# Kernel tuning notes

Measured on AMD Instinct MI355X. Metric: run time of the kernel, lower is better.

The kernel has to match this reference:

```python
import jax, jax.numpy as jnp
import numpy as np

N, E, D, H, A = 50000, 800000, 128, 256, 16


def setup_inputs() -> dict:
    key = jax.random.key(0)
    ks = jax.random.split(key, 16)
    s = 0.05
    return {
        "x": jax.random.normal(ks[0], (N, D), jnp.float32),
        "edge_index": jax.random.randint(ks[1], (2, E), 0, N, dtype=jnp.int32),
        "edge_attr": jax.random.normal(ks[2], (E, A), jnp.float32),
        # GCNConv 1 (input_dim -> hidden_dim): lin weight (no bias) + conv bias
        "W1": jax.random.normal(ks[3], (D, H), jnp.float32) * s,
        "b1": jnp.zeros((H,), jnp.float32),
        # GCNConv 2 (hidden_dim -> input_dim)
        "W2": jax.random.normal(ks[4], (H, D), jnp.float32) * s,
        "b2": jnp.zeros((D,), jnp.float32),
        # output_layer MLP: D -> H -> D
        "Wo1": jax.random.normal(ks[5], (D, H), jnp.float32) * s,
        "bo1": jnp.zeros((H,), jnp.float32),
        "Wo2": jax.random.normal(ks[6], (H, D), jnp.float32) * s,
        "bo2": jnp.zeros((D,), jnp.float32),
        # edge_predictor MLP: 2D+A -> H -> A
        "We1": jax.random.normal(ks[7], (2 * D + A, H), jnp.float32) * s,
        "be1": jnp.zeros((H,), jnp.float32),
        "We2": jax.random.normal(ks[8], (H, A), jnp.float32) * s,
        "be2": jnp.zeros((A,), jnp.float32),
    }


def reference(x, edge_index, edge_attr, W1, b1, W2, b2, Wo1, bo1, Wo2, bo2,
              We1, be1, We2, be2):
    n = x.shape[0]
    row, col = edge_index[0], edge_index[1]
    # GCNConv default: add self-loops, symmetric normalization deg^-1/2 A deg^-1/2
    loop = jnp.arange(n, dtype=row.dtype)
    row_f = jnp.concatenate([row, loop])
    col_f = jnp.concatenate([col, loop])
    deg = jax.ops.segment_sum(jnp.ones_like(col_f, dtype=x.dtype), col_f,
                              num_segments=n)
    dinv = jnp.where(deg > 0, jax.lax.rsqrt(jnp.maximum(deg, 1.0)), 0.0)
    norm = dinv[row_f] * dinv[col_f]  # [E+N]

    def gcn(h, W, b):
        h = h @ W                                # [n, out]
        msg = h[row_f] * norm[:, None]           # gather + scale
        agg = jax.ops.segment_sum(msg, col_f, num_segments=n)  # scatter-add
        return agg + b

    h = jax.nn.relu(gcn(x, W1, b1))
    h = jax.nn.relu(gcn(h, W2, b2))
    h = jax.nn.relu(h @ Wo1 + bo1) @ Wo2 + bo2   # output_layer MLP

    # edge predictor: gather endpoint features, concat with edge_attr, MLP
    edge_input = jnp.concatenate([h[row], h[col], edge_attr], axis=1)
    ea = jax.nn.relu(edge_input @ We1 + be1) @ We2 + be2
    return h, ea
```

## Files before the change

### kernel.cpp

```cpp
#include <hip/hip_runtime.h>
#include <hip/hip_bf16.h>

#define N_NODES 50000
#define N_EDGES 800000
#define DIM_D   128
#define DIM_H   256
#define DIM_A   16

typedef unsigned short u16;
typedef __attribute__((ext_vector_type(4))) float f4;
typedef __attribute__((ext_vector_type(8))) short s8;
typedef __attribute__((ext_vector_type(4))) short s4;

__device__ __forceinline__ u16 f2bf(float f) {
    union { float f; unsigned u; } v; v.f = f;
    unsigned r = v.u + 0x7FFFu + ((v.u >> 16) & 1u);
    return (u16)(r >> 16);
}
__device__ __forceinline__ float bf2f(u16 s) {
    union { unsigned u; float f; } v; v.u = ((unsigned)s) << 16; return v.f;
}
__device__ __forceinline__ s8 zero_s8() {
    s8 v;
#pragma unroll
    for (int i = 0; i < 8; i++) v[i] = 0;
    return v;
}

__device__ __forceinline__ int pq_off(int mt, int q) {
    return (mt >> 2) * 64 + ((mt >> 1) & 1) * 32 + q * 8 + (mt & 1) * 4;
}

__global__ __launch_bounds__(256) void k_zero(int* __restrict__ cnt) {
    int i = blockIdx.x * 256 + threadIdx.x;
    if (i < N_NODES) cnt[i] = 0;
}
__global__ __launch_bounds__(256) void k_count(const int* __restrict__ coli, int* __restrict__ cnt) {
    int e = blockIdx.x * 256 + threadIdx.x;
    if (e < N_EDGES) atomicAdd(&cnt[coli[e]], 1);
}
__global__ __launch_bounds__(256) void k_dinv(const int* __restrict__ cnt, float* __restrict__ dinv) {
    int i = blockIdx.x * 256 + threadIdx.x;
    if (i < N_NODES) dinv[i] = rsqrtf((float)(cnt[i] + 1));
}

#define SCAN_C 49
__global__ __launch_bounds__(1024) void k_scan(const int* __restrict__ cnt, int* __restrict__ start) {
    __shared__ int ps[1024];
    int t = threadIdx.x;
    int base = t * SCAN_C;
    int sum = 0;
    for (int i = 0; i < SCAN_C; i++) {
        int idx = base + i;
        sum += (idx < N_NODES) ? cnt[idx] : 0;
    }
    ps[t] = sum;
    __syncthreads();
    for (int ofs = 1; ofs < 1024; ofs <<= 1) {
        int v = (t >= ofs) ? ps[t - ofs] : 0;
        __syncthreads();
        ps[t] += v;
        __syncthreads();
    }
    int run = (t > 0) ? ps[t - 1] : 0;
    for (int i = 0; i < SCAN_C; i++) {
        int idx = base + i;
        if (idx < N_NODES) {
            start[idx] = run;
            run += cnt[idx];
        }
    }
    if (t == 1023) start[N_NODES] = ps[1023];
}
__global__ __launch_bounds__(256) void k_copy(const int* __restrict__ start, int* __restrict__ cursor) {
    int i = blockIdx.x * 256 + threadIdx.x;
    if (i < N_NODES) cursor[i] = start[i];
}
__global__ __launch_bounds__(256) void k_fill(const int* __restrict__ rowi, const int* __restrict__ coli,
                                              const float* __restrict__ dinv,
                                              int* __restrict__ cursor, int2* __restrict__ pack,
                                              int2* __restrict__ eidx) {
    int e = blockIdx.x * 256 + threadIdx.x;
    if (e >= N_EDGES) return;
    int r = rowi[e], c = coli[e];
    int slot = atomicAdd(&cursor[c], 1);
    float w = dinv[r] * dinv[c];
    pack[slot] = make_int2(r, __float_as_int(w));
    eidx[slot] = make_int2(e, c);
}

__global__ __launch_bounds__(256) void k_cast(const float* __restrict__ X, u16* __restrict__ Y, int n4) {
    int i = blockIdx.x * 256 + threadIdx.x;
    if (i >= n4) return;
    float4 v = *(const float4*)&X[(size_t)i * 4];
    ushort4 o;
    o.x = f2bf(v.x); o.y = f2bf(v.y); o.z = f2bf(v.z); o.w = f2bf(v.w);
    *(ushort4*)&Y[(size_t)i * 4] = o;
}

__global__ __launch_bounds__(256) void k_gather(const u16* __restrict__ X,
                                                const int2* __restrict__ pack,
                                                const int* __restrict__ start,
                                                const float* __restrict__ dinv,
                                                float* __restrict__ z) {
    int node = blockIdx.x * 4 + (threadIdx.x >> 6);
    if (node >= N_NODES) return;
    int lane = threadIdx.x & 63;
    int half = lane >> 5, j = lane & 31;
    int c4 = j * 4;
    float di = dinv[node];
    f4 acc = {0.f, 0.f, 0.f, 0.f};
    if (half == 0) {
        float sl = di * di;
        ushort4 u = *(const ushort4*)&X[(size_t)node * DIM_D + c4];
        acc[0] = bf2f(u.x) * sl; acc[1] = bf2f(u.y) * sl;
        acc[2] = bf2f(u.z) * sl; acc[3] = bf2f(u.w) * sl;
    }
    int s = start[node], e = start[node + 1];
#pragma unroll 8
    for (int i = s + half; i < e; i += 2) {
        int2 p = pack[i];
        float w = __int_as_float(p.y);
        ushort4 u = *(const ushort4*)&X[(size_t)p.x * DIM_D + c4];
        acc[0] += bf2f(u.x) * w; acc[1] += bf2f(u.y) * w;
        acc[2] += bf2f(u.z) * w; acc[3] += bf2f(u.w) * w;
    }
    float t0 = acc[0] + __shfl(acc[0], j + 32);
    float t1 = acc[1] + __shfl(acc[1], j + 32);
    float t2 = acc[2] + __shfl(acc[2], j + 32);
    float t3 = acc[3] + __shfl(acc[3], j + 32);
    if (half == 0)
        *(float4*)&z[(size_t)node * DIM_D + c4] = make_float4(t0, t1, t2, t3);
}

__global__ __launch_bounds__(256) void k_twt(const float* __restrict__ W, u16* __restrict__ Wt,
                                             int K, int Nn) {
    int idx = blockIdx.x * 256 + threadIdx.x;
    if (idx >= K * Nn) return;
    int k = idx / Nn, n = idx - k * Nn;
    Wt[n * K + k] = f2bf(W[idx]);
}

__global__ __launch_bounds__(256) void k_bpq(const float* __restrict__ be1, float* __restrict__ bpq) {
    int i = blockIdx.x * 256 + threadIdx.x;
    if (i < 512) bpq[i] = (i < 256) ? be1[i] : 0.f;
}

#define BM 128
#define BN 64
#define BK 32
#define BKP 56

template <bool A_BF16, bool PRE_BR, bool POST_RELU, bool OUT_BF16, bool PERM_PQ>
__global__ __launch_bounds__(256) void k_gemm(const void* __restrict__ Ap,
                                              const u16* __restrict__ Wt,
                                              const float* __restrict__ preB,
                                              const float* __restrict__ postB,
                                              void* __restrict__ Cp,
                                              int M, int K, int Nn) {
    __shared__ __align__(16) u16 As[BM * BKP];
    __shared__ __align__(16) u16 Bs[BN * BKP];
    const int tid = threadIdx.x;
    const int wid = tid >> 6, lane = tid & 63;
    const int q = lane >> 4, l = lane & 15;
    const int bm = blockIdx.x * BM, bn = blockIdx.y * BN;

    f4 acc[8];
#pragma unroll
    for (int i = 0; i < 8; i++) { f4 zz = {0.f, 0.f, 0.f, 0.f}; acc[i] = zz; }

    for (int k0 = 0; k0 < K; k0 += BK) {
        __syncthreads();
        {
            int n = tid >> 2, kc = (tid & 3) * 8;
            *(int4*)&Bs[n * BKP + kc] = *(const int4*)&Wt[(size_t)(bn + n) * K + k0 + kc];
        }
        if (A_BF16) {
            const u16* A = (const u16*)Ap;
#pragma unroll
            for (int p = 0; p < 2; p++) {
                int m = (tid >> 2) + p * 64, kc = (tid & 3) * 8;
                int gm = bm + m; if (gm >= M) gm = M - 1;
                *(int4*)&As[m * BKP + kc] = *(const int4*)&A[(size_t)gm * K + k0 + kc];
            }
        } else {
            const float* A = (const float*)Ap;
#pragma unroll
            for (int p = 0; p < 4; p++) {
                int m = (tid >> 3) + p * 32, k4 = (tid & 7) * 4;
                int gm = bm + m; if (gm >= M) gm = M - 1;
                float4 v = *(const float4*)&A[(size_t)gm * K + k0 + k4];
                if (PRE_BR) {
                    const float4 pb = *(const float4*)&preB[k0 + k4];
                    v.x = fmaxf(v.x + pb.x, 0.f);
                    v.y = fmaxf(v.y + pb.y, 0.f);
                    v.z = fmaxf(v.z + pb.z, 0.f);
                    v.w = fmaxf(v.w + pb.w, 0.f);
                }
                ushort4 o;
                o.x = f2bf(v.x); o.y = f2bf(v.y); o.z = f2bf(v.z); o.w = f2bf(v.w);
                *(ushort4*)&As[m * BKP + k4] = o;
            }
        }
        __syncthreads();

        s8 af[2], bf[4];
#pragma unroll
        for (int mt = 0; mt < 2; mt++)
            af[mt] = *(const s8*)&As[(wid * 32 + mt * 16 + l) * BKP + q * 8];
#pragma unroll
        for (int nt = 0; nt < 4; nt++)
            bf[nt] = *(const s8*)&Bs[(nt * 16 + l) * BKP + q * 8];
#pragma unroll
        for (int mt = 0; mt < 2; mt++)
#pragma unroll
            for (int nt = 0; nt < 4; nt++)
                acc[mt * 4 + nt] = __builtin_amdgcn_mfma_f32_16x16x32_bf16(
                    af[mt], bf[nt], acc[mt * 4 + nt], 0, 0, 0);
    }

#pragma unroll
    for (int mt = 0; mt < 2; mt++) {
#pragma unroll
        for (int nt = 0; nt < 4; nt++) {
            int colg = bn + nt * 16 + l;
            float pb = postB ? postB[colg] : 0.0f;
            int cols = colg;
            if (PERM_PQ) {
                int w = colg & 63, mtL = w >> 4;
                cols = (colg & ~63) | (((mtL >> 1) & 1) * 32) | (((w >> 2) & 3) * 8)
                       | ((mtL & 1) * 4) | (w & 3);
            }
#pragma unroll
            for (int r = 0; r < 4; r++) {
                int rowg = bm + wid * 32 + mt * 16 + q * 4 + r;
                if (rowg < M) {
                    float v = acc[mt * 4 + nt][r] + pb;
                    if (POST_RELU) v = fmaxf(v, 0.f);
                    if (OUT_BF16)
                        ((u16*)Cp)[(size_t)rowg * Nn + cols] = f2bf(v);
                    else
                        ((float*)Cp)[(size_t)rowg * Nn + cols] = v;
                }
            }
        }
    }
}

#if __has_builtin(__builtin_amdgcn_mfma_f32_16x16x16bf16_1k)
#define KEEP4(a,b,c,d) asm volatile("" :: "v"(a), "v"(b), "v"(c), "v"(d))
__global__ __launch_bounds__(256) void k_edge(const u16* __restrict__ PQ,
                                              const float* __restrict__ attr,
                                              const int2* __restrict__ pack,
                                              const int2* __restrict__ eidx,
                                              const u16* __restrict__ Wct,
                                              const u16* __restrict__ We2t,
                                              const float* __restrict__ be2,
                                              float* __restrict__ outp) {
    const int tid = threadIdx.x, wid = tid >> 6, lane = tid & 63;
    const int q = lane >> 4, l = lane & 15;
    const float4 be2v = *(const float4*)&be2[q * 4];
    const int NT = N_EDGES / 16;
    const int step = gridDim.x * 4;

    s4 we2f[16], wcf[16];
#pragma unroll
    for (int mt = 0; mt < 16; mt++) {
        we2f[mt] = *(const s4*)&We2t[(size_t)l * DIM_H + mt * 16 + q * 4];
        wcf[mt]  = *(const s4*)&Wct[(mt * 16 + l) * 16 + q * 4];
    }

    int tile = blockIdx.x * 4 + wid;
    if (tile >= NT) return;
    int2 pk = pack[tile * 16 + l];
    int2 ec = eidx[tile * 16 + l];

    for (; tile < NT; tile += step) {
        const int re = pk.x, e = ec.x, ce = ec.y;
        const u16* prow = PQ + (size_t)re * 512 + q * 8;
        const u16* qrow = PQ + (size_t)ce * 512 + 256 + q * 8;

        float4 av = *(const float4*)&attr[(size_t)e * DIM_A + q * 4];
        s8 pw[8], qw[8];
#pragma unroll
        for (int w = 0; w < 8; w++) {
            pw[w] = *(const s8*)(prow + w * 32);
            qw[w] = *(const s8*)(qrow + w * 32);
        }
        int ntile = tile + step;
        int ns = (ntile < NT) ? ntile * 16 + l : l;
        int2 pk_n = pack[ns];
        int2 ec_n = eidx[ns];
        KEEP4(pw[0], pw[1], pw[2], pw[3]);
        KEEP4(pw[4], pw[5], pw[6], pw[7]);
        KEEP4(qw[0], qw[1], qw[2], qw[3]);
        KEEP4(qw[4], qw[5], qw[6], qw[7]);
        __builtin_amdgcn_sched_barrier(0);

        s4 af;
        af[0] = (short)f2bf(av.x); af[1] = (short)f2bf(av.y);
        af[2] = (short)f2bf(av.z); af[3] = (short)f2bf(av.w);

        f4 acc2 = {0.f, 0.f, 0.f, 0.f};
#pragma unroll
        for (int w = 0; w < 8; w++) {
#pragma unroll
            for (int s = 0; s < 2; s++) {
                const int mt = w * 2 + s;
                f4 cz = {0.f, 0.f, 0.f, 0.f};
                f4 acc = __builtin_amdgcn_mfma_f32_16x16x16bf16_1k(wcf[mt], af, cz, 0, 0, 0);
                float t0 = bf2f((u16)pw[w][s * 4 + 0]) + bf2f((u16)qw[w][s * 4 + 0]) + acc[0];
                float t1 = bf2f((u16)pw[w][s * 4 + 1]) + bf2f((u16)qw[w][s * 4 + 1]) + acc[1];
                float t2 = bf2f((u16)pw[w][s * 4 + 2]) + bf2f((u16)qw[w][s * 4 + 2]) + acc[2];
                float t3 = bf2f((u16)pw[w][s * 4 + 3]) + bf2f((u16)qw[w][s * 4 + 3]) + acc[3];
                s4 uf;
                uf[0] = (short)f2bf(fmaxf(t0, 0.f));
                uf[1] = (short)f2bf(fmaxf(t1, 0.f));
                uf[2] = (short)f2bf(fmaxf(t2, 0.f));
                uf[3] = (short)f2bf(fmaxf(t3, 0.f));
                acc2 = __builtin_amdgcn_mfma_f32_16x16x16bf16_1k(we2f[mt], uf, acc2, 0, 0, 0);
            }
        }
        *(float4*)&outp[(size_t)e * DIM_A + q * 4] =
            make_float4(acc2[0] + be2v.x, acc2[1] + be2v.y,
                        acc2[2] + be2v.z, acc2[3] + be2v.w);
        pk = pk_n; ec = ec_n;
    }
}
#else
#define UPAD 268
__global__ __launch_bounds__(256) void k_edge(const u16* __restrict__ PQ,
                                              const float* __restrict__ attr,
                                              const int2* __restrict__ pack,
                                              const int2* __restrict__ eidx,
                                              const u16* __restrict__ Wct,
                                              const u16* __restrict__ We2t,
                                              const float* __restrict__ be2,
                                              float* __restrict__ outp) {
    __shared__ __align__(16) u16 ub[4][16][UPAD];
    const int tid = threadIdx.x, wid = tid >> 6, lane = tid & 63;
    const int q = lane >> 4, l = lane & 15;
    const float4 be2v = *(const float4*)&be2[q * 4];
    u16(*u)[UPAD] = ub[wid];

    s8 wcf[16];
#pragma unroll
    for (int mt = 0; mt < 16; mt++) {
        wcf[mt] = zero_s8();
        if (q < 2) wcf[mt] = *(const s8*)&Wct[(mt * 16 + l) * 16 + q * 8];
    }

    for (int tile = blockIdx.x * 4 + wid; tile < N_EDGES / 16; tile += gridDim.x * 4) {
        const int s = tile * 16 + l;
        const int2 pk = pack[s];
        const int2 ec = eidx[s];
        const int re = pk.x, e = ec.x, ce = ec.y;
        const u16* prow = PQ + (size_t)re * 512;
        const u16* qrow = PQ + (size_t)ce * 512 + 256;

        s8 af = zero_s8();
        if (q < 2) {
            const float* ap = &attr[(size_t)e * DIM_A + q * 8];
            float4 a0 = *(const float4*)ap;
            float4 a1 = *(const float4*)(ap + 4);
            af[0] = (short)f2bf(a0.x); af[1] = (short)f2bf(a0.y);
            af[2] = (short)f2bf(a0.z); af[3] = (short)f2bf(a0.w);
            af[4] = (short)f2bf(a1.x); af[5] = (short)f2bf(a1.y);
            af[6] = (short)f2bf(a1.z); af[7] = (short)f2bf(a1.w);
        }

#pragma unroll
        for (int mt = 0; mt < 16; mt++) {
            f4 cz = {0.f, 0.f, 0.f, 0.f};
            f4 acc = __builtin_amdgcn_mfma_f32_16x16x32_bf16(wcf[mt], af, cz, 0, 0, 0);
            ushort4 pu = *(const ushort4*)(prow + pq_off(mt, q));
            ushort4 qu = *(const ushort4*)(qrow + pq_off(mt, q));
            float t0 = bf2f(pu.x) + bf2f(qu.x) + acc[0];
            float t1 = bf2f(pu.y) + bf2f(qu.y) + acc[1];
            float t2 = bf2f(pu.z) + bf2f(qu.z) + acc[2];
            float t3 = bf2f(pu.w) + bf2f(qu.w) + acc[3];
            ushort4 o;
            o.x = f2bf(fmaxf(t0, 0.f)); o.y = f2bf(fmaxf(t1, 0.f));
            o.z = f2bf(fmaxf(t2, 0.f)); o.w = f2bf(fmaxf(t3, 0.f));
            *(ushort4*)&u[l][mt * 16 + q * 4] = o;
        }

        f4 acc2 = {0.f, 0.f, 0.f, 0.f};
#pragma unroll
        for (int ks = 0; ks < 8; ks++) {
            s8 uf = *(const s8*)&u[l][ks * 32 + q * 8];
            s8 wf = *(const s8*)&We2t[(size_t)l * DIM_H + ks * 32 + q * 8];
            acc2 = __builtin_amdgcn_mfma_f32_16x16x32_bf16(wf, uf, acc2, 0, 0, 0);
        }
        *(float4*)&outp[(size_t)e * DIM_A + q * 4] =
            make_float4(acc2[0] + be2v.x, acc2[1] + be2v.y,
                        acc2[2] + be2v.z, acc2[3] + be2v.w);
    }
}
#endif

extern "C" void kernel_launch(void* const* d_in, const int* in_sizes, int n_in,
                              void* d_out, int out_size, void* d_ws, size_t ws_size,
                              hipStream_t stream) {
    (void)in_sizes; (void)n_in; (void)out_size; (void)ws_size;
    const float* x    = (const float*)d_in[0];
    const int*   ei   = (const int*)d_in[1];
    const float* attr = (const float*)d_in[2];
    const float* W1   = (const float*)d_in[3];
    const float* b1   = (const float*)d_in[4];
    const float* W2   = (const float*)d_in[5];
    const float* b2   = (const float*)d_in[6];
    const float* Wo1  = (const float*)d_in[7];
    const float* bo1  = (const float*)d_in[8];
    const float* Wo2  = (const float*)d_in[9];
    const float* bo2  = (const float*)d_in[10];
    const float* We1  = (const float*)d_in[11];
    const float* be1  = (const float*)d_in[12];
    const float* We2  = (const float*)d_in[13];
    const float* be2  = (const float*)d_in[14];
    const int* rowi = ei;
    const int* coli = ei + N_EDGES;

    float* hout = (float*)d_out;
    float* eout = hout + (size_t)N_NODES * DIM_D;

    char* ws = (char*)d_ws;
    size_t off = 0;
    auto nxt = [&](size_t b) -> void* {
        void* p = ws + off; off = (off + b + 255) & ~(size_t)255; return p;
    };
    float* dinv = (float*)nxt((size_t)N_NODES * 4);
    int* cnt    = (int*)nxt((size_t)N_NODES * 4);
    int* startp = (int*)nxt((size_t)(N_NODES + 1) * 4);
    int* cursor = (int*)nxt((size_t)N_NODES * 4);
    int2* pack  = (int2*)nxt((size_t)N_EDGES * 8);
    int2* eidx  = (int2*)nxt((size_t)N_EDGES * 8);
    u16* W1t   = (u16*)nxt(128 * 256 * 2);
    u16* W2t   = (u16*)nxt(128 * 256 * 2);
    u16* Wo1t  = (u16*)nxt(128 * 256 * 2);
    u16* Wo2t  = (u16*)nxt(128 * 256 * 2);
    u16* Wabt  = (u16*)nxt(512 * 128 * 2);
    u16* Wct   = (u16*)nxt(256 * 16 * 2);
    u16* We2t  = (u16*)nxt(16 * 256 * 2);
    float* bpq = (float*)nxt(512 * 4);
    u16* xb    = (u16*)nxt((size_t)N_NODES * DIM_D * 2);
    float* z   = (float*)nxt((size_t)N_NODES * DIM_D * 4);
    u16* h1    = (u16*)nxt((size_t)N_NODES * DIM_H * 2);
    u16* yb    = (u16*)nxt((size_t)N_NODES * DIM_D * 2);
    u16* PQb = (u16*)z;

    const int gN = (N_NODES + 255) / 256;
    const int gE = (N_EDGES + 255) / 256;

    k_twt<<<(128 * 256 + 255) / 256, 256, 0, stream>>>(W1, W1t, 128, 256);
    k_twt<<<(128 * 256 + 255) / 256, 256, 0, stream>>>(W2, W2t, 256, 128);
    k_twt<<<(128 * 256 + 255) / 256, 256, 0, stream>>>(Wo1, Wo1t, 128, 256);
    k_twt<<<(128 * 256 + 255) / 256, 256, 0, stream>>>(Wo2, Wo2t, 256, 128);
    k_twt<<<(128 * 256 + 255) / 256, 256, 0, stream>>>(We1, Wabt, 128, 256);
    k_twt<<<(128 * 256 + 255) / 256, 256, 0, stream>>>(We1 + 128 * 256, Wabt + 256 * 128, 128, 256);
    k_twt<<<(16 * 256 + 255) / 256, 256, 0, stream>>>(We1 + 256 * 256, Wct, 16, 256);
    k_twt<<<(16 * 256 + 255) / 256, 256, 0, stream>>>(We2, We2t, 256, 16);
    k_bpq<<<2, 256, 0, stream>>>(be1, bpq);

    k_zero<<<gN, 256, 0, stream>>>(cnt);
    k_count<<<gE, 256, 0, stream>>>(coli, cnt);
    k_dinv<<<gN, 256, 0, stream>>>(cnt, dinv);
    k_scan<<<1, 1024, 0, stream>>>(cnt, startp);
    k_copy<<<gN, 256, 0, stream>>>(startp, cursor);
    k_fill<<<gE, 256, 0, stream>>>(rowi, coli, dinv, cursor, pack, eidx);

    k_cast<<<(N_NODES * DIM_D / 4 + 255) / 256, 256, 0, stream>>>(x, xb, N_NODES * DIM_D / 4);

    dim3 g4(391, 4), g2(391, 2), g8(391, 8);
    const int gG = (N_NODES + 3) / 4;
    k_gather<<<gG, 256, 0, stream>>>(xb, pack, startp, dinv, z);
    k_gemm<false, false, true, true, false><<<g4, 256, 0, stream>>>(z, W1t, nullptr, b1, h1, N_NODES, 128, 256);
    k_gemm<true, false, false, true, false><<<g2, 256, 0, stream>>>(h1, W2t, nullptr, nullptr, yb, N_NODES, 256, 128);
    k_gather<<<gG, 256, 0, stream>>>(yb, pack, startp, dinv, z);
    k_gemm<false, true, true, true, false><<<g4, 256, 0, stream>>>(z, Wo1t, b2, bo1, h1, N_NODES, 128, 256);
    k_gemm<true, false, false, false, false><<<g2, 256, 0, stream>>>(h1, Wo2t, nullptr, bo2, hout, N_NODES, 256, 128);
    k_gemm<false, false, false, true, true><<<g8, 256, 0, stream>>>(hout, Wabt, nullptr, bpq, PQb, N_NODES, 128, 512);
    k_edge<<<2048, 256, 0, stream>>>(PQb, attr, pack, eidx, Wct, We2t, be2, eout);
}
```

Baseline: 681.2 us.

## Split gather edge ranges per half-wave, stage edge MLP weights in LDS

The GCN gather kernel now gives each half-wave a contiguous half of the node's edge range and unrolls by four with loads issued ahead of the FMAs, raising memory-level parallelism. The edge kernel moves the 32 per-lane weight fragments from registers into shared memory and reads them per MFMA, cutting VGPR pressure to allow more waves in flight. It also feeds the P+Q sum straight in as the MFMA accumulator input, removing separate adds. The cost is extra LDS reads inside the hot loop.

New measurement: 667.1 us. -2.1%, faster.

```diff
diff --git a/kernel.cpp b/kernel.cpp
--- a/kernel.cpp
+++ b/kernel.cpp
@@ -116,9 +116,28 @@
         acc[0] = bf2f(u.x) * sl; acc[1] = bf2f(u.y) * sl;
         acc[2] = bf2f(u.z) * sl; acc[3] = bf2f(u.w) * sl;
     }
-    int s = start[node], e = start[node + 1];
-#pragma unroll 8
-    for (int i = s + half; i < e; i += 2) {
+    int s0 = start[node], e0 = start[node + 1];
+    int h0 = (e0 - s0 + 1) >> 1;
+    int i   = half ? (s0 + h0) : s0;
+    int end = half ? e0 : (s0 + h0);
+    for (; i + 3 < end; i += 4) {
+        int2 p0 = pack[i], p1 = pack[i + 1], p2 = pack[i + 2], p3 = pack[i + 3];
+        ushort4 u0 = *(const ushort4*)&X[(size_t)p0.x * DIM_D + c4];
+        ushort4 u1 = *(const ushort4*)&X[(size_t)p1.x * DIM_D + c4];
+        ushort4 u2 = *(const ushort4*)&X[(size_t)p2.x * DIM_D + c4];
+        ushort4 u3 = *(const ushort4*)&X[(size_t)p3.x * DIM_D + c4];
+        float w0 = __int_as_float(p0.y), w1 = __int_as_float(p1.y);
+        float w2 = __int_as_float(p2.y), w3 = __int_as_float(p3.y);
+        acc[0] += bf2f(u0.x) * w0; acc[1] += bf2f(u0.y) * w0;
+        acc[2] += bf2f(u0.z) * w0; acc[3] += bf2f(u0.w) * w0;
+        acc[0] += bf2f(u1.x) * w1; acc[1] += bf2f(u1.y) * w1;
+        acc[2] += bf2f(u1.z) * w1; acc[3] += bf2f(u1.w) * w1;
+        acc[0] += bf2f(u2.x) * w2; acc[1] += bf2f(u2.y) * w2;
+        acc[2] += bf2f(u2.z) * w2; acc[3] += bf2f(u2.w) * w2;
+        acc[0] += bf2f(u3.x) * w3; acc[1] += bf2f(u3.y) * w3;
+        acc[2] += bf2f(u3.z) * w3; acc[3] += bf2f(u3.w) * w3;
+    }
+    for (; i < end; i++) {
         int2 p = pack[i];
         float w = __int_as_float(p.y);
         ushort4 u = *(const ushort4*)&X[(size_t)p.x * DIM_D + c4];
@@ -257,18 +276,21 @@
                                               const u16* __restrict__ We2t,
                                               const float* __restrict__ be2,
                                               float* __restrict__ outp) {
+    __shared__ __align__(16) u16 lwc[16 * 64 * 4];
+    __shared__ __align__(16) u16 lwe[16 * 64 * 4];
     const int tid = threadIdx.x, wid = tid >> 6, lane = tid & 63;
     const int q = lane >> 4, l = lane & 15;
+    for (int u = tid; u < 1024; u += 256) {
+        int smt = u >> 6, sl = (u >> 2) & 15, sq = u & 3;
+        *(uint2*)&lwc[u * 4] = *(const uint2*)&Wct[(smt * 16 + sl) * 16 + sq * 4];
+        *(uint2*)&lwe[u * 4] = *(const uint2*)&We2t[sl * DIM_H + smt * 16 + sq * 4];
+    }
+    __syncthreads();
+
     const float4 be2v = *(const float4*)&be2[q * 4];
     const int NT = N_EDGES / 16;
     const int step = gridDim.x * 4;
-
-    s4 we2f[16], wcf[16];
-#pragma unroll
-    for (int mt = 0; mt < 16; mt++) {
-        we2f[mt] = *(const s4*)&We2t[(size_t)l * DIM_H + mt * 16 + q * 4];
-        wcf[mt]  = *(const s4*)&Wct[(mt * 16 + l) * 16 + q * 4];
-    }
+    const int fbase = (l * 4 + q) * 4;
 
     int tile = blockIdx.x * 4 + wid;
     if (tile >= NT) return;
@@ -307,18 +329,20 @@
 #pragma unroll
             for (int s = 0; s < 2; s++) {
                 const int mt = w * 2 + s;
-                f4 cz = {0.f, 0.f, 0.f, 0.f};
-                f4 acc = __builtin_amdgcn_mfma_f32_16x16x16bf16_1k(wcf[mt], af, cz, 0, 0, 0);
-                float t0 = bf2f((u16)pw[w][s * 4 + 0]) + bf2f((u16)qw[w][s * 4 + 0]) + acc[0];
-                float t1 = bf2f((u16)pw[w][s * 4 + 1]) + bf2f((u16)qw[w][s * 4 + 1]) + acc[1];
-                float t2 = bf2f((u16)pw[w][s * 4 + 2]) + bf2f((u16)qw[w][s * 4 + 2]) + acc[2];
-                float t3 = bf2f((u16)pw[w][s * 4 + 3]) + bf2f((u16)qw[w][s * 4 + 3]) + acc[3];
+                s4 wcf = *(const s4*)&lwc[mt * 256 + fbase];
+                f4 pqs;
+                pqs[0] = bf2f((u16)pw[w][s * 4 + 0]) + bf2f((u16)qw[w][s * 4 + 0]);
+                pqs[1] = bf2f((u16)pw[w][s * 4 + 1]) + bf2f((u16)qw[w][s * 4 + 1]);
+                pqs[2] = bf2f((u16)pw[w][s * 4 + 2]) + bf2f((u16)qw[w][s * 4 + 2]);
+                pqs[3] = bf2f((u16)pw[w][s * 4 + 3]) + bf2f((u16)qw[w][s * 4 + 3]);
+                f4 acc = __builtin_amdgcn_mfma_f32_16x16x16bf16_1k(wcf, af, pqs, 0, 0, 0);
                 s4 uf;
-                uf[0] = (short)f2bf(fmaxf(t0, 0.f));
-                uf[1] = (short)f2bf(fmaxf(t1, 0.f));
-                uf[2] = (short)f2bf(fmaxf(t2, 0.f));
-                uf[3] = (short)f2bf(fmaxf(t3, 0.f));
-                acc2 = __builtin_amdgcn_mfma_f32_16x16x16bf16_1k(we2f[mt], uf, acc2, 0, 0, 0);
+                uf[0] = (short)f2bf(fmaxf(acc[0], 0.f));
+                uf[1] = (short)f2bf(fmaxf(acc[1], 0.f));
+                uf[2] = (short)f2bf(fmaxf(acc[2], 0.f));
+                uf[3] = (short)f2bf(fmaxf(acc[3], 0.f));
+                s4 wef = *(const s4*)&lwe[mt * 256 + fbase];
+                acc2 = __builtin_amdgcn_mfma_f32_16x16x16bf16_1k(wef, uf, acc2, 0, 0, 0);
             }
         }
         *(float4*)&outp[(size_t)e * DIM_A + q * 4] =
```
